# Kernel optimization log

Measured on AMD Instinct MI355X. Metric: run time of the kernel, lower is better.

Reference implementation:

```python
import jax, jax.numpy as jnp
import numpy as np

TINY = np.finfo(np.float32).tiny


def setup_inputs() -> dict:
    key = jax.random.key(0)
    k1, k2, k3 = jax.random.split(key, 3)
    B, IN, OUT = 4096, 4096, 1024
    x = jax.random.normal(k1, (B, IN), dtype=jnp.float32)
    weight = jax.random.normal(k2, (IN, OUT), dtype=jnp.float32)
    uniform = jax.random.uniform(k3, (IN, OUT), dtype=jnp.float32)
    T = jnp.ones((1,), dtype=jnp.float32)
    return {"x": x, "weight": weight, "uniform": uniform, "T": T}


def reference(x, weight, uniform, T):
    # training-path forward of ConcreteLayer
    # uniform -> (1 - tiny) * u + tiny, then Gumbel noise
    u = (1.0 - TINY) * uniform + TINY
    gumbel = -jnp.log(-jnp.log(u))                      # [in, out]
    noisy_logits = (weight + gumbel) / T                # temperature scaling
    samples = jax.nn.softmax(noisy_logits, axis=1)      # softmax over out dim (torch default for 2D)
    out = jnp.einsum('bi,ik->bk', x, samples)           # [batch, out]
    return out
```

## Files before the change

kernel.cpp:

```cpp
#include <hip/hip_runtime.h>
#include <cstdint>
#include <cstddef>


#define TINYF 1.17549435082228750797e-38f

typedef unsigned short u16;
typedef __attribute__((ext_vector_type(8))) short bf16x8;
typedef __attribute__((ext_vector_type(4))) float f32x4;

__device__ __forceinline__ u16 f2bf(float f) {
  union { float f; uint32_t u; } v; v.f = f;
  uint32_t r = v.u + 0x7FFFu + ((v.u >> 16) & 1u);
  return (u16)(r >> 16);
}

__device__ __forceinline__ void gld_lds16(const void* g, void* l) {
  __builtin_amdgcn_global_load_lds(
      (__attribute__((address_space(1))) void*)(g),
      (__attribute__((address_space(3))) void*)(l), 16, 0, 0);
}

__global__ void cast_x_kernel(const float4* __restrict__ x, ushort4* __restrict__ xb, int n4) {
  int i = blockIdx.x * blockDim.x + threadIdx.x;
  if (i >= n4) return;
  float4 v = x[i];
  ushort4 o;
  o.x = f2bf(v.x); o.y = f2bf(v.y); o.z = f2bf(v.z); o.w = f2bf(v.w);
  xb[i] = o;
}

__global__ void softmax_stats_kernel(const float* __restrict__ W, const float* __restrict__ U,
                                     const float* __restrict__ Tp, float2* __restrict__ stats) {
  const int row = blockIdx.x;
  const int t = threadIdx.x;
  const float invT = 1.0f / Tp[0];
  float lg[4];
#pragma unroll
  for (int j = 0; j < 4; ++j) {
    int c = t + j * 256;
    size_t gi = (size_t)row * 1024 + c;
    float uu = U[gi] * (1.0f - TINYF) + TINYF;
    float g = -logf(-logf(uu));
    lg[j] = (W[gi] + g) * invT;
  }
  float m = fmaxf(fmaxf(lg[0], lg[1]), fmaxf(lg[2], lg[3]));
#pragma unroll
  for (int o = 32; o > 0; o >>= 1) m = fmaxf(m, __shfl_down(m, o));
  __shared__ float redm[4], reds[4];
  if ((t & 63) == 0) redm[t >> 6] = m;
  __syncthreads();
  m = fmaxf(fmaxf(redm[0], redm[1]), fmaxf(redm[2], redm[3]));
  float s = 0.f;
#pragma unroll
  for (int j = 0; j < 4; ++j) s += expf(lg[j] - m);
#pragma unroll
  for (int o = 32; o > 0; o >>= 1) s += __shfl_down(s, o);
  if ((t & 63) == 0) reds[t >> 6] = s;
  __syncthreads();
  if (t == 0) stats[row] = make_float2(m, reds[0] + reds[1] + reds[2] + reds[3]);
}

__global__ void norm_transpose_kernel(const float* __restrict__ W, const float* __restrict__ U,
                                      const float* __restrict__ Tp, const float2* __restrict__ stats,
                                      u16* __restrict__ BT) {
  __shared__ float tile[64][65];
  const int k0 = blockIdx.x * 64, n0 = blockIdx.y * 64;
  const int t = threadIdx.x;
  const float invT = 1.0f / Tp[0];
  {
    const int nn = t & 63, kq = t >> 6;
#pragma unroll
    for (int r = 0; r < 16; ++r) {
      int kk = r * 4 + kq;
      size_t gi = (size_t)(k0 + kk) * 1024 + (n0 + nn);
      float uu = U[gi] * (1.0f - TINYF) + TINYF;
      float g = -logf(-logf(uu));
      float lgv = (W[gi] + g) * invT;
      float2 st = stats[k0 + kk];
      tile[kk][nn] = expf(lgv - st.x) * (1.0f / st.y);
    }
  }
  __syncthreads();
  {
    const int kk = t & 63, nq = t >> 6;
#pragma unroll
    for (int r = 0; r < 16; ++r) {
      int nn = r * 4 + nq;
      BT[(size_t)(n0 + nn) * 4096 + (k0 + kk)] = f2bf(tile[kk][nn]);
    }
  }
}

#define TILE_M 128
#define TILE_N 64
#define TILE_K 32

__launch_bounds__(256)
__global__ void gemm_bt_kernel(const u16* __restrict__ A, const u16* __restrict__ BT,
                               float* __restrict__ C, int M, int N, int K) {
  __shared__ u16 As[TILE_M * TILE_K];
  __shared__ u16 Bs[TILE_N * TILE_K];

  const int tid = threadIdx.x;
  const int lane = tid & 63, w = tid >> 6;
  const int wm = w >> 1, wn = w & 1;
  const int m0 = blockIdx.x * TILE_M, n0 = blockIdx.y * TILE_N;
  const int quad = lane >> 4, r16 = lane & 15;
  const int lrow = lane >> 2;
  const int lk = (lane & 3) * 8;

  f32x4 acc[4][2] = {};

  for (int kt = 0; kt < K; kt += TILE_K) {
    __syncthreads();
#pragma unroll
    for (int c = 0; c < 2; ++c) {
      int chunk = w * 2 + c;
      int row = chunk * 16 + lrow;
      gld_lds16(A + (size_t)(m0 + row) * K + kt + lk, (char*)As + chunk * 1024);
    }
    {
      int row = w * 16 + lrow;
      gld_lds16(BT + (size_t)(n0 + row) * K + kt + lk, (char*)Bs + w * 1024);
    }
    __syncthreads();

    bf16x8 aF[4], bF[2];
#pragma unroll
    for (int mi = 0; mi < 4; ++mi)
      aF[mi] = *(const bf16x8*)&As[(wm * 64 + mi * 16 + r16) * TILE_K + quad * 8];
#pragma unroll
    for (int ni = 0; ni < 2; ++ni)
      bF[ni] = *(const bf16x8*)&Bs[(wn * 32 + ni * 16 + r16) * TILE_K + quad * 8];
#pragma unroll
    for (int mi = 0; mi < 4; ++mi)
#pragma unroll
      for (int ni = 0; ni < 2; ++ni)
        acc[mi][ni] = __builtin_amdgcn_mfma_f32_16x16x32_bf16(aF[mi], bF[ni], acc[mi][ni], 0, 0, 0);
  }

#pragma unroll
  for (int mi = 0; mi < 4; ++mi)
#pragma unroll
    for (int ni = 0; ni < 2; ++ni)
#pragma unroll
      for (int r = 0; r < 4; ++r) {
        int row = m0 + wm * 64 + mi * 16 + quad * 4 + r;
        int col = n0 + wn * 32 + ni * 16 + r16;
        C[(size_t)row * N + col] = acc[mi][ni][r];
      }
}

extern "C" void kernel_launch(void* const* d_in, const int* in_sizes, int n_in,
                              void* d_out, int out_size, void* d_ws, size_t ws_size,
                              hipStream_t stream) {
  const int M = 4096, K = 4096, N = 1024;
  const float* x = (const float*)d_in[0];
  const float* W = (const float*)d_in[1];
  const float* U = (const float*)d_in[2];
  const float* Tp = (const float*)d_in[3];
  float* out = (float*)d_out;

  char* ws = (char*)d_ws;
  u16* xb = (u16*)ws;
  u16* bt = (u16*)(ws + (size_t)M * K * 2);
  float2* stats = (float2*)(ws + (size_t)M * K * 2 + (size_t)N * K * 2);

  cast_x_kernel<<<dim3((M * K / 4) / 256), 256, 0, stream>>>((const float4*)x, (ushort4*)xb, M * K / 4);
  softmax_stats_kernel<<<dim3(K), 256, 0, stream>>>(W, U, Tp, stats);
  norm_transpose_kernel<<<dim3(K / 64, N / 64), 256, 0, stream>>>(W, U, Tp, stats, bt);
  gemm_bt_kernel<<<dim3(M / TILE_M, N / TILE_N), 256, 0, stream>>>(xb, bt, out, M, N, K);
}
```

Before: 217.8 us.

## Use hardware log/exp, vectorize softmax passes, enlarge GEMM tile with split-K atomics

Gumbel noise and the softmax exponentials now use the hardware log2/exp2 intrinsics in place of libm logf/expf. The stats and normalize-transpose kernels switch to float4 loads and ushort4 stores. The GEMM tile grows from 128x64 to 128x128 and K is split in two across blockIdx.z, with partial sums combined through atomicAdd into an output that a new kernel zeroes first. This trades transcendental cost and launch shape for an extra zeroing pass, atomic write traffic, and slightly lower-precision math.

```diff
diff --git a/kernel.cpp b/kernel.cpp
--- a/kernel.cpp
+++ b/kernel.cpp
@@ -4,6 +4,8 @@
 
 
 #define TINYF 1.17549435082228750797e-38f
+#define LN2F 0.69314718055994530942f
+#define LOG2EF 1.44269504088896340736f
 
 typedef unsigned short u16;
 typedef __attribute__((ext_vector_type(8))) short bf16x8;
@@ -15,10 +17,24 @@
   return (u16)(r >> 16);
 }
 
+__device__ __forceinline__ float log2_hw(float x) { return __builtin_amdgcn_logf(x); }
+__device__ __forceinline__ float exp2_hw(float x) { return __builtin_amdgcn_exp2f(x); }
+
+__device__ __forceinline__ float gumbel_fast(float u) {
+  float t = -log2_hw(u);
+  return -LN2F * log2_hw(t * LN2F);
+}
+__device__ __forceinline__ float exp_fast(float x) { return exp2_hw(x * LOG2EF); }
+
 __device__ __forceinline__ void gld_lds16(const void* g, void* l) {
   __builtin_amdgcn_global_load_lds(
       (__attribute__((address_space(1))) void*)(g),
       (__attribute__((address_space(3))) void*)(l), 16, 0, 0);
+}
+
+__global__ void zero_kernel(float4* __restrict__ p, int n4) {
+  int i = blockIdx.x * blockDim.x + threadIdx.x;
+  if (i < n4) p[i] = make_float4(0.f, 0.f, 0.f, 0.f);
 }
 
 __global__ void cast_x_kernel(const float4* __restrict__ x, ushort4* __restrict__ xb, int n4) {
@@ -30,20 +46,18 @@
   xb[i] = o;
 }
 
-__global__ void softmax_stats_kernel(const float* __restrict__ W, const float* __restrict__ U,
+__global__ void softmax_stats_kernel(const float4* __restrict__ W4, const float4* __restrict__ U4,
                                      const float* __restrict__ Tp, float2* __restrict__ stats) {
   const int row = blockIdx.x;
   const int t = threadIdx.x;
   const float invT = 1.0f / Tp[0];
+  size_t gi = (size_t)row * 256 + t;
+  float4 w = W4[gi], u = U4[gi];
   float lg[4];
-#pragma unroll
-  for (int j = 0; j < 4; ++j) {
-    int c = t + j * 256;
-    size_t gi = (size_t)row * 1024 + c;
-    float uu = U[gi] * (1.0f - TINYF) + TINYF;
-    float g = -logf(-logf(uu));
-    lg[j] = (W[gi] + g) * invT;
-  }
+  lg[0] = (w.x + gumbel_fast(u.x * (1.0f - TINYF) + TINYF)) * invT;
+  lg[1] = (w.y + gumbel_fast(u.y * (1.0f - TINYF) + TINYF)) * invT;
+  lg[2] = (w.z + gumbel_fast(u.z * (1.0f - TINYF) + TINYF)) * invT;
+  lg[3] = (w.w + gumbel_fast(u.w * (1.0f - TINYF) + TINYF)) * invT;
   float m = fmaxf(fmaxf(lg[0], lg[1]), fmaxf(lg[2], lg[3]));
 #pragma unroll
   for (int o = 32; o > 0; o >>= 1) m = fmaxf(m, __shfl_down(m, o));
@@ -51,9 +65,7 @@
   if ((t & 63) == 0) redm[t >> 6] = m;
   __syncthreads();
   m = fmaxf(fmaxf(redm[0], redm[1]), fmaxf(redm[2], redm[3]));
-  float s = 0.f;
-#pragma unroll
-  for (int j = 0; j < 4; ++j) s += expf(lg[j] - m);
+  float s = exp_fast(lg[0] - m) + exp_fast(lg[1] - m) + exp_fast(lg[2] - m) + exp_fast(lg[3] - m);
 #pragma unroll
   for (int o = 32; o > 0; o >>= 1) s += __shfl_down(s, o);
   if ((t & 63) == 0) reds[t >> 6] = s;
@@ -69,86 +81,99 @@
   const int t = threadIdx.x;
   const float invT = 1.0f / Tp[0];
   {
-    const int nn = t & 63, kq = t >> 6;
-#pragma unroll
-    for (int r = 0; r < 16; ++r) {
-      int kk = r * 4 + kq;
-      size_t gi = (size_t)(k0 + kk) * 1024 + (n0 + nn);
-      float uu = U[gi] * (1.0f - TINYF) + TINYF;
-      float g = -logf(-logf(uu));
-      float lgv = (W[gi] + g) * invT;
+    const int nn4 = (t & 15) * 4, kq = t >> 4;
+#pragma unroll
+    for (int r = 0; r < 4; ++r) {
+      int kk = r * 16 + kq;
+      size_t gi = (size_t)(k0 + kk) * 1024 + (n0 + nn4);
+      float4 w = *(const float4*)&W[gi];
+      float4 u = *(const float4*)&U[gi];
       float2 st = stats[k0 + kk];
-      tile[kk][nn] = expf(lgv - st.x) * (1.0f / st.y);
+      float rs = 1.0f / st.y;
+      tile[kk][nn4 + 0] = exp_fast((w.x + gumbel_fast(u.x * (1.0f - TINYF) + TINYF)) * invT - st.x) * rs;
+      tile[kk][nn4 + 1] = exp_fast((w.y + gumbel_fast(u.y * (1.0f - TINYF) + TINYF)) * invT - st.x) * rs;
+      tile[kk][nn4 + 2] = exp_fast((w.z + gumbel_fast(u.z * (1.0f - TINYF) + TINYF)) * invT - st.x) * rs;
+      tile[kk][nn4 + 3] = exp_fast((w.w + gumbel_fast(u.w * (1.0f - TINYF) + TINYF)) * invT - st.x) * rs;
     }
   }
   __syncthreads();
   {
-    const int kk = t & 63, nq = t >> 6;
-#pragma unroll
-    for (int r = 0; r < 16; ++r) {
-      int nn = r * 4 + nq;
-      BT[(size_t)(n0 + nn) * 4096 + (k0 + kk)] = f2bf(tile[kk][nn]);
+    const int kk4 = (t & 15) * 4, nq = t >> 4;
+#pragma unroll
+    for (int r = 0; r < 4; ++r) {
+      int nn = r * 16 + nq;
+      ushort4 o;
+      o.x = f2bf(tile[kk4 + 0][nn]);
+      o.y = f2bf(tile[kk4 + 1][nn]);
+      o.z = f2bf(tile[kk4 + 2][nn]);
+      o.w = f2bf(tile[kk4 + 3][nn]);
+      *(ushort4*)&BT[(size_t)(n0 + nn) * 4096 + (k0 + kk4)] = o;
     }
   }
 }
 
-#define TILE_M 128
-#define TILE_N 64
-#define TILE_K 32
+#define TM 128
+#define TN 128
+#define TK 32
 
 __launch_bounds__(256)
 __global__ void gemm_bt_kernel(const u16* __restrict__ A, const u16* __restrict__ BT,
                                float* __restrict__ C, int M, int N, int K) {
-  __shared__ u16 As[TILE_M * TILE_K];
-  __shared__ u16 Bs[TILE_N * TILE_K];
+  __shared__ u16 As[TM * TK];
+  __shared__ u16 Bs[TN * TK];
 
   const int tid = threadIdx.x;
   const int lane = tid & 63, w = tid >> 6;
   const int wm = w >> 1, wn = w & 1;
-  const int m0 = blockIdx.x * TILE_M, n0 = blockIdx.y * TILE_N;
+  const int m0 = blockIdx.x * TM, n0 = blockIdx.y * TN;
   const int quad = lane >> 4, r16 = lane & 15;
   const int lrow = lane >> 2;
   const int lk = (lane & 3) * 8;
 
-  f32x4 acc[4][2] = {};
-
-  for (int kt = 0; kt < K; kt += TILE_K) {
+  const int kz = blockIdx.z;
+  const int Kh = K >> 1;
+  const u16* Ak = A + (size_t)kz * Kh;
+  const u16* Bk = BT + (size_t)kz * Kh;
+
+  f32x4 acc[4][4] = {};
+
+  for (int kt = 0; kt < Kh; kt += TK) {
     __syncthreads();
 #pragma unroll
     for (int c = 0; c < 2; ++c) {
       int chunk = w * 2 + c;
-      int row = chunk * 16 + lrow;
-      gld_lds16(A + (size_t)(m0 + row) * K + kt + lk, (char*)As + chunk * 1024);
-    }
-    {
-      int row = w * 16 + lrow;
-      gld_lds16(BT + (size_t)(n0 + row) * K + kt + lk, (char*)Bs + w * 1024);
+      gld_lds16(Ak + (size_t)(m0 + chunk * 16 + lrow) * K + kt + lk, (char*)As + chunk * 1024);
+    }
+#pragma unroll
+    for (int c = 0; c < 2; ++c) {
+      int chunk = w * 2 + c;
+      gld_lds16(Bk + (size_t)(n0 + chunk * 16 + lrow) * K + kt + lk, (char*)Bs + chunk * 1024);
     }
     __syncthreads();
 
-    bf16x8 aF[4], bF[2];
+    bf16x8 aF[4], bF[4];
 #pragma unroll
     for (int mi = 0; mi < 4; ++mi)
-      aF[mi] = *(const bf16x8*)&As[(wm * 64 + mi * 16 + r16) * TILE_K + quad * 8];
-#pragma unroll
-    for (int ni = 0; ni < 2; ++ni)
-      bF[ni] = *(const bf16x8*)&Bs[(wn * 32 + ni * 16 + r16) * TILE_K + quad * 8];
+      aF[mi] = *(const bf16x8*)&As[(wm * 64 + mi * 16 + r16) * TK + quad * 8];
+#pragma unroll
+    for (int ni = 0; ni < 4; ++ni)
+      bF[ni] = *(const bf16x8*)&Bs[(wn * 64 + ni * 16 + r16) * TK + quad * 8];
 #pragma unroll
     for (int mi = 0; mi < 4; ++mi)
 #pragma unroll
-      for (int ni = 0; ni < 2; ++ni)
+      for (int ni = 0; ni < 4; ++ni)
         acc[mi][ni] = __builtin_amdgcn_mfma_f32_16x16x32_bf16(aF[mi], bF[ni], acc[mi][ni], 0, 0, 0);
   }
 
 #pragma unroll
   for (int mi = 0; mi < 4; ++mi)
 #pragma unroll
-    for (int ni = 0; ni < 2; ++ni)
+    for (int ni = 0; ni < 4; ++ni)
 #pragma unroll
       for (int r = 0; r < 4; ++r) {
         int row = m0 + wm * 64 + mi * 16 + quad * 4 + r;
-        int col = n0 + wn * 32 + ni * 16 + r16;
-        C[(size_t)row * N + col] = acc[mi][ni][r];
+        int col = n0 + wn * 64 + ni * 16 + r16;
+        atomicAdd(&C[(size_t)row * N + col], acc[mi][ni][r]);
       }
 }
 
@@ -167,8 +192,9 @@
   u16* bt = (u16*)(ws + (size_t)M * K * 2);
   float2* stats = (float2*)(ws + (size_t)M * K * 2 + (size_t)N * K * 2);
 
+  zero_kernel<<<dim3((M * N / 4 + 255) / 256), 256, 0, stream>>>((float4*)out, M * N / 4);
   cast_x_kernel<<<dim3((M * K / 4) / 256), 256, 0, stream>>>((const float4*)x, (ushort4*)xb, M * K / 4);
-  softmax_stats_kernel<<<dim3(K), 256, 0, stream>>>(W, U, Tp, stats);
+  softmax_stats_kernel<<<dim3(K), 256, 0, stream>>>((const float4*)W, (const float4*)U, Tp, stats);
   norm_transpose_kernel<<<dim3(K / 64, N / 64), 256, 0, stream>>>(W, U, Tp, stats, bt);
-  gemm_bt_kernel<<<dim3(M / TILE_M, N / TILE_N), 256, 0, stream>>>(xb, bt, out, M, N, K);
-}
+  gemm_bt_kernel<<<dim3(M / TM, N / TN, 2), 256, 0, stream>>>(xb, bt, out, M, N, K);
+}
```

New measurement: 217.1 us. No clear change (-0.3%).
